# Performance work log

Hardware: AMD Instinct MI355X
Metric: run time of the kernel (lower is better)

Reference implementation:

```python
import jax, jax.numpy as jnp
import numpy as np

MODEL_DIM = 768
N_HEAD = 12
HEAD_DIM = MODEL_DIM // N_HEAD
B, S = 2, 2048


def setup_inputs() -> dict:
    key = jax.random.key(0)
    ks = jax.random.split(key, 11)
    sc = 1.0 / np.sqrt(MODEL_DIM)
    inp = {
        "q": jax.random.normal(ks[0], (B, S, MODEL_DIM), jnp.float32),
        "k": jax.random.normal(ks[1], (B, S, MODEL_DIM), jnp.float32),
        "v": jax.random.normal(ks[2], (B, S, MODEL_DIM), jnp.float32),
        "wq_w": jax.random.normal(ks[3], (MODEL_DIM, MODEL_DIM), jnp.float32) * sc,
        "wq_b": jax.random.normal(ks[4], (MODEL_DIM,), jnp.float32) * sc,
        "wk_w": jax.random.normal(ks[5], (MODEL_DIM, MODEL_DIM), jnp.float32) * sc,
        "wk_b": jax.random.normal(ks[6], (MODEL_DIM,), jnp.float32) * sc,
        "wv_w": jax.random.normal(ks[7], (MODEL_DIM, MODEL_DIM), jnp.float32) * sc,
        "wv_b": jax.random.normal(ks[8], (MODEL_DIM,), jnp.float32) * sc,
        "wo_w": jax.random.normal(ks[9], (MODEL_DIM, MODEL_DIM), jnp.float32) * sc,
        "wo_b": jax.random.normal(ks[10], (MODEL_DIM,), jnp.float32) * sc,
    }
    return inp


def _split_heads(x):
    b, s, _ = x.shape
    return x.reshape(b, s, N_HEAD, HEAD_DIM).transpose(0, 2, 1, 3)  # [B,H,S,Dh]


def reference(q, k, v, wq_w, wq_b, wk_w, wk_b, wv_w, wv_b, wo_w, wo_b):
    # Linear projections (torch Linear: x @ W.T + b)
    query = _split_heads(q @ wq_w.T + wq_b)
    key = _split_heads(k @ wk_w.T + wk_b)
    value = _split_heads(v @ wv_w.T + wv_b)
    scale = 1.0 / np.sqrt(HEAD_DIM)
    scores = jnp.einsum("bhqd,bhkd->bhqk", query, key) * scale
    attn_weights = jax.nn.softmax(scores, axis=-1)
    context = jnp.einsum("bhqk,bhkd->bhqd", attn_weights, value)
    b, h, s, dh = context.shape
    context = context.transpose(0, 2, 1, 3).reshape(b, s, MODEL_DIM)
    output = context @ wo_w.T + wo_b
    return output, attn_weights
```

## Files before the change

### kernel.cpp

```cpp
#include <hip/hip_runtime.h>
#include <stdint.h>

#define S_LEN   2048
#define NH      12
#define NBH     24
#define DMODEL  768
#define OUT0    3145728
#define SD      131072
#define WSZ     589824

#define QB_OFF   0
#define KB_OFF   3145728
#define VB_OFF   6291456
#define WQ_OFF   9437184
#define WK_OFF   10027008
#define WV_OFF   10616832
#define WO_OFF   11206656
#define QH_OFF   11796480
#define KH_OFF   14942208
#define VT_OFF   18087936
#define CTX_OFF  21233664

typedef __attribute__((ext_vector_type(4))) float          f32x4;
typedef __attribute__((ext_vector_type(8))) __bf16         bf16x8;
typedef __attribute__((ext_vector_type(4))) __bf16         bf16x4;
typedef __attribute__((ext_vector_type(4))) float          fl4;
typedef __attribute__((ext_vector_type(4))) unsigned short us4;

__device__ __forceinline__ unsigned short f2bf(float f) {
  union { float f; unsigned u; } x; x.f = f;
  return (unsigned short)((x.u + 0x7FFFu + ((x.u >> 16) & 1u)) >> 16);
}

__device__ __forceinline__ float fexp2(float x) {
#if __has_builtin(__builtin_amdgcn_exp2f)
  return __builtin_amdgcn_exp2f(x);
#else
  return exp2f(x);
#endif
}

__device__ __forceinline__ void gld16(const void* g, void* l) {
  __builtin_amdgcn_global_load_lds((__attribute__((address_space(1))) void*)g,
                                   (__attribute__((address_space(3))) void*)l,
                                   16, 0, 0);
}

#define MFMA(a, b, c) __builtin_amdgcn_mfma_f32_16x16x32_bf16((a), (b), (c), 0, 0, 0)
#define MEMBAR() asm volatile("" ::: "memory")
#define SBAR()   __builtin_amdgcn_s_barrier()

__global__ __launch_bounds__(256) void cvt_kernel(
    const float* __restrict__ q, const float* __restrict__ k, const float* __restrict__ v,
    const float* __restrict__ wq, const float* __restrict__ wk, const float* __restrict__ wv,
    const float* __restrict__ wo, unsigned short* __restrict__ ws)
{
  const int seg = blockIdx.y;
  const float* src; unsigned short* dst; int n; float sc = 1.0f;
  if      (seg == 0) { src = q;  dst = ws + QB_OFF; n = OUT0; }
  else if (seg == 1) { src = k;  dst = ws + KB_OFF; n = OUT0; }
  else if (seg == 2) { src = v;  dst = ws + VB_OFF; n = OUT0; }
  else if (seg == 3) { src = wq; dst = ws + WQ_OFF; n = WSZ; sc = 0.125f; }
  else if (seg == 4) { src = wk; dst = ws + WK_OFF; n = WSZ; }
  else if (seg == 5) { src = wv; dst = ws + WV_OFF; n = WSZ; }
  else               { src = wo; dst = ws + WO_OFF; n = WSZ; }
  const int i4 = blockIdx.x * blockDim.x + threadIdx.x;
  if (i4 * 4 >= n) return;
  fl4 f = ((const fl4*)src)[i4];
  us4 o;
  o.x = f2bf(f.x * sc); o.y = f2bf(f.y * sc);
  o.z = f2bf(f.z * sc); o.w = f2bf(f.w * sc);
  ((us4*)dst)[i4] = o;
}

__global__ __launch_bounds__(256, 2) void proj_qkv(
    unsigned short* __restrict__ ws, const float* __restrict__ bq,
    const float* __restrict__ bk, const float* __restrict__ bv)
{
  __shared__ __align__(16) unsigned short As[2][8192];
  __shared__ __align__(16) unsigned short Bs[2][8192];
  const int mat = blockIdx.z;
  const unsigned short* X = ws + (size_t)mat * OUT0;
  const unsigned short* W = ws + WQ_OFF + (size_t)mat * WSZ;
  const float* bias = (mat == 0) ? bq : ((mat == 1) ? bk : bv);
  const float bsc = (mat == 0) ? 0.125f : 1.0f;
  unsigned short* dst = ws + QH_OFF + (size_t)mat * OUT0;
  const int m0 = blockIdx.y * 128, n0 = blockIdx.x * 128;
  const int tid = threadIdx.x, lane = tid & 63, w = tid >> 6;
  const int wm = w >> 1, wn = w & 1, qd = lane >> 4, ln = lane & 15;
  const int srow = lane >> 3, sc8 = ((lane & 7) ^ srow) * 8;

#pragma unroll
  for (int i = 0; i < 4; i++) {
    const int row = (w * 4 + i) * 8 + srow;
    gld16(X + (size_t)(m0 + row) * 768 + sc8, &As[0][(w * 4 + i) * 512]);
    gld16(W + (size_t)(n0 + row) * 768 + sc8, &Bs[0][(w * 4 + i) * 512]);
  }

  f32x4 acc[4][4] = {};
  for (int kk = 0; kk < 12; kk++) {
    const int knx = (kk == 11) ? 0 : (kk + 1);
    const int nb = (kk + 1) & 1;
#pragma unroll
    for (int i = 0; i < 4; i++) {
      const int row = (w * 4 + i) * 8 + srow;
      gld16(X + (size_t)(m0 + row) * 768 + knx * 64 + sc8, &As[nb][(w * 4 + i) * 512]);
      gld16(W + (size_t)(n0 + row) * 768 + knx * 64 + sc8, &Bs[nb][(w * 4 + i) * 512]);
    }
    asm volatile("s_waitcnt vmcnt(8)" ::: "memory");
    SBAR();
    const unsigned short* Ac = As[kk & 1];
    const unsigned short* Bc = Bs[kk & 1];
    bf16x8 a[4][2], b[4][2];
#pragma unroll
    for (int kst = 0; kst < 2; kst++) {
#pragma unroll
      for (int mt = 0; mt < 4; mt++)
        a[mt][kst] = *(const bf16x8*)(Ac + (wm * 64 + mt * 16 + ln) * 64 + (((kst * 4 + qd) ^ (ln & 7)) * 8));
#pragma unroll
      for (int nt = 0; nt < 4; nt++)
        b[nt][kst] = *(const bf16x8*)(Bc + (wn * 64 + nt * 16 + ln) * 64 + (((kst * 4 + qd) ^ (ln & 7)) * 8));
    }
#pragma unroll
    for (int mt = 0; mt < 4; mt++)
#pragma unroll
      for (int nt = 0; nt < 4; nt++) {
        acc[mt][nt] = MFMA(a[mt][0], b[nt][0], acc[mt][nt]);
        acc[mt][nt] = MFMA(a[mt][1], b[nt][1], acc[mt][nt]);
      }
    MEMBAR();
    SBAR();
  }
#pragma unroll
  for (int nt = 0; nt < 4; nt++) {
    const int n = n0 + wn * 64 + nt * 16 + ln;
    const float bvv = bias[n] * bsc;
    const int h = n >> 6, d = n & 63;
    if (mat < 2) {
#pragma unroll
      for (int mt = 0; mt < 4; mt++)
#pragma unroll
        for (int r = 0; r < 4; r++) {
          const int m = m0 + wm * 64 + mt * 16 + qd * 4 + r;
          const int bb = m >> 11, s = m & 2047;
          dst[(size_t)(bb * NH + h) * SD + (size_t)s * 64 + d] = f2bf(acc[mt][nt][r] + bvv);
        }
    } else {
#pragma unroll
      for (int mt = 0; mt < 4; mt++) {
        const int m = m0 + wm * 64 + mt * 16 + qd * 4;
        const int bb = m >> 11, s = m & 2047;
        us4 o;
        o.x = f2bf(acc[mt][nt][0] + bvv); o.y = f2bf(acc[mt][nt][1] + bvv);
        o.z = f2bf(acc[mt][nt][2] + bvv); o.w = f2bf(acc[mt][nt][3] + bvv);
        *(us4*)(dst + (size_t)(bb * NH + h) * SD + (size_t)d * S_LEN + s) = o;
      }
    }
  }
  asm volatile("s_waitcnt vmcnt(0)" ::: "memory");
}

__global__ __launch_bounds__(256, 2) void attn_kernel(
    unsigned short* __restrict__ ws, float* __restrict__ attn_out)
{
  __shared__ __align__(16) unsigned short lds[40960];
  unsigned short* K0 = lds;
  unsigned short* K1 = lds + 8192;
  unsigned short* Vt = lds + 16384;
  unsigned short* P  = lds + 24576;
  float* rsum        = (float*)(lds + 24576);
  unsigned short* Qs = lds + 32768;

  const int bh = blockIdx.y;
  const int i0 = blockIdx.x * 128;
  const unsigned short* Qg = ws + QH_OFF + (size_t)bh * SD + (size_t)i0 * 64;
  const unsigned short* Kg = ws + KH_OFF + (size_t)bh * SD;
  const unsigned short* Vg = ws + VT_OFF + (size_t)bh * SD;
  float* attnB = attn_out + (size_t)bh * S_LEN * S_LEN + (size_t)i0 * S_LEN;
  unsigned short* ctxB = ws + CTX_OFF + ((size_t)(bh / NH) * S_LEN + i0) * DMODEL + (bh % NH) * 64;

  const int tid = threadIdx.x, lane = tid & 63, w = tid >> 6;
  const int wm = w >> 1, wn = w & 1, qd = lane >> 4, ln = lane & 15;
  const int srow = lane >> 3, sc8 = ((lane & 7) ^ srow) * 8;
  const float LOG2E = 1.4426950408889634f;

#pragma unroll
  for (int i = 0; i < 4; i++) {
    const int row = (w * 4 + i) * 8 + srow;
    gld16(Qg + (size_t)row * 64 + sc8, Qs + (w * 4 + i) * 512);
  }
  MEMBAR();
#pragma unroll
  for (int i = 0; i < 4; i++) {
    const int row = (w * 4 + i) * 8 + srow;
    gld16(Kg + (size_t)row * 64 + sc8, K0 + (w * 4 + i) * 512);
  }
  if (tid < 128) rsum[tid] = 0.f;
  asm volatile("s_waitcnt vmcnt(4) lgkmcnt(0)" ::: "memory");
  SBAR();

  bf16x8 bq[4][2];
#pragma unroll
  for (int kst = 0; kst < 2; kst++)
#pragma unroll
    for (int qt = 0; qt < 4; qt++)
      bq[qt][kst] = *(const bf16x8*)(Qs + (wm * 64 + qt * 16 + ln) * 64 + (((kst * 4 + qd) ^ (ln & 7)) * 8));

  float psl[4] = {0.f, 0.f, 0.f, 0.f};
  for (int jt = 0; jt < 16; jt++) {
    const unsigned short* Kn = Kg + (size_t)((jt + 1) & 15) * 8192;
    unsigned short* Kw = (jt & 1) ? K0 : K1;
#pragma unroll
    for (int i = 0; i < 4; i++) {
      const int row = (w * 4 + i) * 8 + srow;
      gld16(Kn + (size_t)row * 64 + sc8, Kw + (w * 4 + i) * 512);
    }
    asm volatile("s_waitcnt vmcnt(4)" ::: "memory");
    SBAR();
    const unsigned short* Kc = (jt & 1) ? K1 : K0;
    bf16x8 ak[4][2];
#pragma unroll
    for (int kst = 0; kst < 2; kst++)
#pragma unroll
      for (int kt = 0; kt < 4; kt++)
        ak[kt][kst] = *(const bf16x8*)(Kc + (wn * 64 + kt * 16 + ln) * 64 + (((kst * 4 + qd) ^ (ln & 7)) * 8));
#pragma unroll
    for (int qt = 0; qt < 4; qt++)
#pragma unroll
      for (int kt = 0; kt < 4; kt++) {
        f32x4 c = {0.f, 0.f, 0.f, 0.f};
        c = MFMA(ak[kt][0], bq[qt][0], c);
        c = MFMA(ak[kt][1], bq[qt][1], c);
        psl[qt] += fexp2(c[0] * LOG2E) + fexp2(c[1] * LOG2E)
                 + fexp2(c[2] * LOG2E) + fexp2(c[3] * LOG2E);
      }
    MEMBAR();
    SBAR();
  }
#pragma unroll
  for (int qt = 0; qt < 4; qt++) {
    float v = psl[qt];
    v += __shfl_xor(v, 16);
    v += __shfl_xor(v, 32);
    psl[qt] = v;
  }
  if (lane < 16) {
#pragma unroll
    for (int qt = 0; qt < 4; qt++)
      atomicAdd(&rsum[wm * 64 + qt * 16 + lane], psl[qt]);
  }
  asm volatile("s_waitcnt lgkmcnt(0)" ::: "memory");
  SBAR();
  float rv[4];
#pragma unroll
  for (int qt = 0; qt < 4; qt++) rv[qt] = 1.0f / rsum[wm * 64 + qt * 16 + ln];

  f32x4 ctx[4][2] = {};
  for (int jt = 0; jt < 16; jt++) {
#pragma unroll
    for (int i = 0; i < 4; i++) {
      const int d = (w * 4 + i) * 4 + qd;
      const int csw = ((lane & 15) ^ ((i & 1) * 4 + qd)) * 8;
      gld16(Vg + (size_t)d * S_LEN + jt * 128 + csw, Vt + (w * 4 + i) * 512);
    }
    MEMBAR();
    const unsigned short* Kn = Kg + (size_t)((jt + 1) & 15) * 8192;
    unsigned short* Kw = (jt & 1) ? K0 : K1;
#pragma unroll
    for (int i = 0; i < 4; i++) {
      const int row = (w * 4 + i) * 8 + srow;
      gld16(Kn + (size_t)row * 64 + sc8, Kw + (w * 4 + i) * 512);
    }
    asm volatile("s_waitcnt vmcnt(8)" ::: "memory");
    SBAR();

    const unsigned short* Kc = (jt & 1) ? K1 : K0;
    bf16x8 ak[4][2];
#pragma unroll
    for (int kst = 0; kst < 2; kst++)
#pragma unroll
      for (int kt = 0; kt < 4; kt++)
        ak[kt][kst] = *(const bf16x8*)(Kc + (wn * 64 + kt * 16 + ln) * 64 + (((kst * 4 + qd) ^ (ln & 7)) * 8));

#pragma unroll
    for (int qt = 0; qt < 4; qt++) {
      const int qrow = wm * 64 + qt * 16 + ln;
      float* aRow = attnB + (size_t)qrow * S_LEN + jt * 128 + wn * 64 + qd * 4;
      unsigned short* pRow = P + qrow * 128;
      const int r7x8 = (ln & 7) * 8;
#pragma unroll
      for (int kt = 0; kt < 4; kt++) {
        f32x4 c = {0.f, 0.f, 0.f, 0.f};
        c = MFMA(ak[kt][0], bq[qt][0], c);
        c = MFMA(ak[kt][1], bq[qt][1], c);
        f32x4 pv;
        pv.x = fexp2(c[0] * LOG2E) * rv[qt];
        pv.y = fexp2(c[1] * LOG2E) * rv[qt];
        pv.z = fexp2(c[2] * LOG2E) * rv[qt];
        pv.w = fexp2(c[3] * LOG2E) * rv[qt];
        *(f32x4*)(aRow + kt * 16) = pv;
        bf16x4 pb;
        pb.x = (__bf16)pv.x; pb.y = (__bf16)pv.y;
        pb.z = (__bf16)pv.z; pb.w = (__bf16)pv.w;
        *(bf16x4*)(pRow + ((wn * 64 + kt * 16 + qd * 4) ^ r7x8)) = pb;
      }
    }
    asm volatile("s_waitcnt vmcnt(20) lgkmcnt(0)" ::: "memory");
    SBAR();
#pragma unroll
    for (int kst = 0; kst < 4; kst++) {
      bf16x8 pa[4], vb[2];
#pragma unroll
      for (int mt = 0; mt < 4; mt++)
        pa[mt] = *(const bf16x8*)(P + (wm * 64 + mt * 16 + ln) * 128 + ((kst * 32 + qd * 8) ^ ((ln & 7) * 8)));
#pragma unroll
      for (int nt = 0; nt < 2; nt++)
        vb[nt] = *(const bf16x8*)(Vt + (wn * 32 + nt * 16 + ln) * 128 + (((kst * 4 + qd) ^ (ln & 7)) * 8));
#pragma unroll
      for (int mt = 0; mt < 4; mt++)
#pragma unroll
        for (int nt = 0; nt < 2; nt++)
          ctx[mt][nt] = MFMA(pa[mt], vb[nt], ctx[mt][nt]);
    }
    MEMBAR();
    SBAR();
  }
#pragma unroll
  for (int mt = 0; mt < 4; mt++)
#pragma unroll
    for (int nt = 0; nt < 2; nt++)
#pragma unroll
      for (int r = 0; r < 4; r++) {
        const int row = wm * 64 + mt * 16 + qd * 4 + r;
        ctxB[(size_t)row * DMODEL + wn * 32 + nt * 16 + ln] = f2bf(ctx[mt][nt][r]);
      }
  asm volatile("s_waitcnt vmcnt(0)" ::: "memory");
}

__global__ __launch_bounds__(256, 2) void out_proj(
    const unsigned short* __restrict__ ws, const float* __restrict__ wob,
    float* __restrict__ out)
{
  __shared__ __align__(16) unsigned short As[2][8192];
  __shared__ __align__(16) unsigned short Bs[2][8192];
  const unsigned short* X = ws + CTX_OFF;
  const unsigned short* W = ws + WO_OFF;
  const int m0 = blockIdx.y * 128, n0 = blockIdx.x * 128;
  const int tid = threadIdx.x, lane = tid & 63, w = tid >> 6;
  const int wm = w >> 1, wn = w & 1, qd = lane >> 4, ln = lane & 15;
  const int srow = lane >> 3, sc8 = ((lane & 7) ^ srow) * 8;

#pragma unroll
  for (int i = 0; i < 4; i++) {
    const int row = (w * 4 + i) * 8 + srow;
    gld16(X + (size_t)(m0 + row) * 768 + sc8, &As[0][(w * 4 + i) * 512]);
    gld16(W + (size_t)(n0 + row) * 768 + sc8, &Bs[0][(w * 4 + i) * 512]);
  }

  f32x4 acc[4][4] = {};
  for (int kk = 0; kk < 12; kk++) {
    const int knx = (kk == 11) ? 0 : (kk + 1);
    const int nb = (kk + 1) & 1;
#pragma unroll
    for (int i = 0; i < 4; i++) {
      const int row = (w * 4 + i) * 8 + srow;
      gld16(X + (size_t)(m0 + row) * 768 + knx * 64 + sc8, &As[nb][(w * 4 + i) * 512]);
      gld16(W + (size_t)(n0 + row) * 768 + knx * 64 + sc8, &Bs[nb][(w * 4 + i) * 512]);
    }
    asm volatile("s_waitcnt vmcnt(8)" ::: "memory");
    SBAR();
    const unsigned short* Ac = As[kk & 1];
    const unsigned short* Bc = Bs[kk & 1];
    bf16x8 a[4][2], b[4][2];
#pragma unroll
    for (int kst = 0; kst < 2; kst++) {
#pragma unroll
      for (int mt = 0; mt < 4; mt++)
        a[mt][kst] = *(const bf16x8*)(Ac + (wm * 64 + mt * 16 + ln) * 64 + (((kst * 4 + qd) ^ (ln & 7)) * 8));
#pragma unroll
      for (int nt = 0; nt < 4; nt++)
        b[nt][kst] = *(const bf16x8*)(Bc + (wn * 64 + nt * 16 + ln) * 64 + (((kst * 4 + qd) ^ (ln & 7)) * 8));
    }
#pragma unroll
    for (int mt = 0; mt < 4; mt++)
#pragma unroll
      for (int nt = 0; nt < 4; nt++) {
        acc[mt][nt] = MFMA(a[mt][0], b[nt][0], acc[mt][nt]);
        acc[mt][nt] = MFMA(a[mt][1], b[nt][1], acc[mt][nt]);
      }
    MEMBAR();
    SBAR();
  }
#pragma unroll
  for (int nt = 0; nt < 4; nt++) {
    const int n = n0 + wn * 64 + nt * 16 + ln;
    const float bvv = wob[n];
#pragma unroll
    for (int mt = 0; mt < 4; mt++)
#pragma unroll
      for (int r = 0; r < 4; r++) {
        const int m = m0 + wm * 64 + mt * 16 + qd * 4 + r;
        out[(size_t)m * DMODEL + n] = acc[mt][nt][r] + bvv;
      }
  }
  asm volatile("s_waitcnt vmcnt(0)" ::: "memory");
}

extern "C" void kernel_launch(void* const* d_in, const int* in_sizes, int n_in,
                              void* d_out, int out_size, void* d_ws, size_t ws_size,
                              hipStream_t stream)
{
  const float* q  = (const float*)d_in[0];
  const float* k  = (const float*)d_in[1];
  const float* v  = (const float*)d_in[2];
  const float* wq = (const float*)d_in[3];
  const float* bq = (const float*)d_in[4];
  const float* wk = (const float*)d_in[5];
  const float* bk = (const float*)d_in[6];
  const float* wv = (const float*)d_in[7];
  const float* bv = (const float*)d_in[8];
  const float* wo = (const float*)d_in[9];
  const float* bo = (const float*)d_in[10];
  unsigned short* ws = (unsigned short*)d_ws;
  float* out = (float*)d_out;

  cvt_kernel<<<dim3(3072, 7), 256, 0, stream>>>(q, k, v, wq, wk, wv, wo, ws);
  proj_qkv<<<dim3(6, 32, 3), 256, 0, stream>>>(ws, bq, bk, bv);
  attn_kernel<<<dim3(16, 24), 256, 0, stream>>>(ws, out + OUT0);
  out_proj<<<dim3(6, 32), 256, 0, stream>>>(ws, bo, out);
}
```

Baseline: 569.0 us.

## Shrink attention tile to 64 query rows and keep P in registers via shuffles

The attention kernel now processes 64 query rows per block instead of 128. Each wave owns 16 full query rows, so row sums reduce within the wave without LDS atomics. The softmax probabilities are packed to bf16 in registers and redistributed with cross-lane shuffles into the MFMA A-operand layout, which removes the P staging buffer in LDS. Q is staged in the Vt buffer, LDS drops from 80KB to 48KB, and launch bounds rise to 3 blocks per CU to raise occupancy. In exchange, each K/V tile loaded from global memory is reused by fewer query rows, doubling K/V traffic, and the kernel adds shuffle overhead.

```diff
diff --git a/kernel.cpp b/kernel.cpp
--- a/kernel.cpp
+++ b/kernel.cpp
@@ -23,7 +23,6 @@
 
 typedef __attribute__((ext_vector_type(4))) float          f32x4;
 typedef __attribute__((ext_vector_type(8))) __bf16         bf16x8;
-typedef __attribute__((ext_vector_type(4))) __bf16         bf16x4;
 typedef __attribute__((ext_vector_type(4))) float          fl4;
 typedef __attribute__((ext_vector_type(4))) unsigned short us4;
 
@@ -160,19 +159,16 @@
   asm volatile("s_waitcnt vmcnt(0)" ::: "memory");
 }
 
-__global__ __launch_bounds__(256, 2) void attn_kernel(
+__global__ __launch_bounds__(256, 3) void attn_kernel(
     unsigned short* __restrict__ ws, float* __restrict__ attn_out)
 {
-  __shared__ __align__(16) unsigned short lds[40960];
+  __shared__ __align__(16) unsigned short lds[24576];
   unsigned short* K0 = lds;
   unsigned short* K1 = lds + 8192;
   unsigned short* Vt = lds + 16384;
-  unsigned short* P  = lds + 24576;
-  float* rsum        = (float*)(lds + 24576);
-  unsigned short* Qs = lds + 32768;
 
   const int bh = blockIdx.y;
-  const int i0 = blockIdx.x * 128;
+  const int i0 = blockIdx.x * 64;
   const unsigned short* Qg = ws + QH_OFF + (size_t)bh * SD + (size_t)i0 * 64;
   const unsigned short* Kg = ws + KH_OFF + (size_t)bh * SD;
   const unsigned short* Vg = ws + VT_OFF + (size_t)bh * SD;
@@ -180,14 +176,14 @@
   unsigned short* ctxB = ws + CTX_OFF + ((size_t)(bh / NH) * S_LEN + i0) * DMODEL + (bh % NH) * 64;
 
   const int tid = threadIdx.x, lane = tid & 63, w = tid >> 6;
-  const int wm = w >> 1, wn = w & 1, qd = lane >> 4, ln = lane & 15;
+  const int qd = lane >> 4, ln = lane & 15;
   const int srow = lane >> 3, sc8 = ((lane & 7) ^ srow) * 8;
   const float LOG2E = 1.4426950408889634f;
 
 #pragma unroll
-  for (int i = 0; i < 4; i++) {
-    const int row = (w * 4 + i) * 8 + srow;
-    gld16(Qg + (size_t)row * 64 + sc8, Qs + (w * 4 + i) * 512);
+  for (int i = 0; i < 2; i++) {
+    const int row = (w * 2 + i) * 8 + srow;
+    gld16(Qg + (size_t)row * 64 + sc8, Vt + (w * 2 + i) * 512);
   }
   MEMBAR();
 #pragma unroll
@@ -195,21 +191,18 @@
     const int row = (w * 4 + i) * 8 + srow;
     gld16(Kg + (size_t)row * 64 + sc8, K0 + (w * 4 + i) * 512);
   }
-  if (tid < 128) rsum[tid] = 0.f;
-  asm volatile("s_waitcnt vmcnt(4) lgkmcnt(0)" ::: "memory");
+  asm volatile("s_waitcnt vmcnt(4)" ::: "memory");
   SBAR();
 
-  bf16x8 bq[4][2];
+  bf16x8 bq[2];
 #pragma unroll
   for (int kst = 0; kst < 2; kst++)
-#pragma unroll
-    for (int qt = 0; qt < 4; qt++)
-      bq[qt][kst] = *(const bf16x8*)(Qs + (wm * 64 + qt * 16 + ln) * 64 + (((kst * 4 + qd) ^ (ln & 7)) * 8));
-
-  float psl[4] = {0.f, 0.f, 0.f, 0.f};
+    bq[kst] = *(const bf16x8*)(Vt + (w * 16 + ln) * 64 + (((kst * 4 + qd) ^ (ln & 7)) * 8));
+
+  float psl = 0.f;
   for (int jt = 0; jt < 16; jt++) {
     const unsigned short* Kn = Kg + (size_t)((jt + 1) & 15) * 8192;
-    unsigned short* Kw = (jt & 1) ? K0 : K1;
+    unsigned short* Kw = ((jt + 1) & 1) ? K1 : K0;
 #pragma unroll
     for (int i = 0; i < 4; i++) {
       const int row = (w * 4 + i) * 8 + srow;
@@ -218,44 +211,28 @@
     asm volatile("s_waitcnt vmcnt(4)" ::: "memory");
     SBAR();
     const unsigned short* Kc = (jt & 1) ? K1 : K0;
-    bf16x8 ak[4][2];
-#pragma unroll
-    for (int kst = 0; kst < 2; kst++)
-#pragma unroll
-      for (int kt = 0; kt < 4; kt++)
-        ak[kt][kst] = *(const bf16x8*)(Kc + (wn * 64 + kt * 16 + ln) * 64 + (((kst * 4 + qd) ^ (ln & 7)) * 8));
-#pragma unroll
-    for (int qt = 0; qt < 4; qt++)
-#pragma unroll
-      for (int kt = 0; kt < 4; kt++) {
-        f32x4 c = {0.f, 0.f, 0.f, 0.f};
-        c = MFMA(ak[kt][0], bq[qt][0], c);
-        c = MFMA(ak[kt][1], bq[qt][1], c);
-        psl[qt] += fexp2(c[0] * LOG2E) + fexp2(c[1] * LOG2E)
-                 + fexp2(c[2] * LOG2E) + fexp2(c[3] * LOG2E);
-      }
-    MEMBAR();
-    SBAR();
-  }
-#pragma unroll
-  for (int qt = 0; qt < 4; qt++) {
-    float v = psl[qt];
-    v += __shfl_xor(v, 16);
-    v += __shfl_xor(v, 32);
-    psl[qt] = v;
-  }
-  if (lane < 16) {
-#pragma unroll
-    for (int qt = 0; qt < 4; qt++)
-      atomicAdd(&rsum[wm * 64 + qt * 16 + lane], psl[qt]);
-  }
-  asm volatile("s_waitcnt lgkmcnt(0)" ::: "memory");
-  SBAR();
-  float rv[4];
-#pragma unroll
-  for (int qt = 0; qt < 4; qt++) rv[qt] = 1.0f / rsum[wm * 64 + qt * 16 + ln];
-
-  f32x4 ctx[4][2] = {};
+#pragma unroll
+    for (int kt = 0; kt < 8; kt++) {
+      bf16x8 ak0 = *(const bf16x8*)(Kc + (kt * 16 + ln) * 64 + ((qd ^ (ln & 7)) * 8));
+      bf16x8 ak1 = *(const bf16x8*)(Kc + (kt * 16 + ln) * 64 + (((4 + qd) ^ (ln & 7)) * 8));
+      f32x4 c = {0.f, 0.f, 0.f, 0.f};
+      c = MFMA(ak0, bq[0], c);
+      c = MFMA(ak1, bq[1], c);
+      psl += fexp2(c[0] * LOG2E) + fexp2(c[1] * LOG2E)
+           + fexp2(c[2] * LOG2E) + fexp2(c[3] * LOG2E);
+    }
+    MEMBAR();
+    SBAR();
+  }
+  psl += __shfl_xor(psl, 16);
+  psl += __shfl_xor(psl, 32);
+  const float rv = 1.0f / psl;
+
+  const int l0 = ((qd & 1) * 2) * 16 + ln;
+  const int l1 = l0 + 16;
+  const bool hi = (qd & 2) != 0;
+
+  f32x4 ctx[4] = {};
   for (int jt = 0; jt < 16; jt++) {
 #pragma unroll
     for (int i = 0; i < 4; i++) {
@@ -265,7 +242,7 @@
     }
     MEMBAR();
     const unsigned short* Kn = Kg + (size_t)((jt + 1) & 15) * 8192;
-    unsigned short* Kw = (jt & 1) ? K0 : K1;
+    unsigned short* Kw = ((jt + 1) & 1) ? K1 : K0;
 #pragma unroll
     for (int i = 0; i < 4; i++) {
       const int row = (w * 4 + i) * 8 + srow;
@@ -275,65 +252,52 @@
     SBAR();
 
     const unsigned short* Kc = (jt & 1) ? K1 : K0;
-    bf16x8 ak[4][2];
-#pragma unroll
-    for (int kst = 0; kst < 2; kst++)
-#pragma unroll
-      for (int kt = 0; kt < 4; kt++)
-        ak[kt][kst] = *(const bf16x8*)(Kc + (wn * 64 + kt * 16 + ln) * 64 + (((kst * 4 + qd) ^ (ln & 7)) * 8));
-
-#pragma unroll
-    for (int qt = 0; qt < 4; qt++) {
-      const int qrow = wm * 64 + qt * 16 + ln;
-      float* aRow = attnB + (size_t)qrow * S_LEN + jt * 128 + wn * 64 + qd * 4;
-      unsigned short* pRow = P + qrow * 128;
-      const int r7x8 = (ln & 7) * 8;
-#pragma unroll
-      for (int kt = 0; kt < 4; kt++) {
-        f32x4 c = {0.f, 0.f, 0.f, 0.f};
-        c = MFMA(ak[kt][0], bq[qt][0], c);
-        c = MFMA(ak[kt][1], bq[qt][1], c);
-        f32x4 pv;
-        pv.x = fexp2(c[0] * LOG2E) * rv[qt];
-        pv.y = fexp2(c[1] * LOG2E) * rv[qt];
-        pv.z = fexp2(c[2] * LOG2E) * rv[qt];
-        pv.w = fexp2(c[3] * LOG2E) * rv[qt];
-        *(f32x4*)(aRow + kt * 16) = pv;
-        bf16x4 pb;
-        pb.x = (__bf16)pv.x; pb.y = (__bf16)pv.y;
-        pb.z = (__bf16)pv.z; pb.w = (__bf16)pv.w;
-        *(bf16x4*)(pRow + ((wn * 64 + kt * 16 + qd * 4) ^ r7x8)) = pb;
-      }
-    }
-    asm volatile("s_waitcnt vmcnt(20) lgkmcnt(0)" ::: "memory");
-    SBAR();
+    unsigned pkx[8], pky[8];
+#pragma unroll
+    for (int kt = 0; kt < 8; kt++) {
+      bf16x8 ak0 = *(const bf16x8*)(Kc + (kt * 16 + ln) * 64 + ((qd ^ (ln & 7)) * 8));
+      bf16x8 ak1 = *(const bf16x8*)(Kc + (kt * 16 + ln) * 64 + (((4 + qd) ^ (ln & 7)) * 8));
+      f32x4 c = {0.f, 0.f, 0.f, 0.f};
+      c = MFMA(ak0, bq[0], c);
+      c = MFMA(ak1, bq[1], c);
+      f32x4 pv;
+      pv.x = fexp2(c[0] * LOG2E) * rv;
+      pv.y = fexp2(c[1] * LOG2E) * rv;
+      pv.z = fexp2(c[2] * LOG2E) * rv;
+      pv.w = fexp2(c[3] * LOG2E) * rv;
+      *(f32x4*)(attnB + (size_t)(w * 16 + ln) * S_LEN + jt * 128 + kt * 16 + qd * 4) = pv;
+      pkx[kt] = (unsigned)f2bf(pv.x) | ((unsigned)f2bf(pv.y) << 16);
+      pky[kt] = (unsigned)f2bf(pv.z) | ((unsigned)f2bf(pv.w) << 16);
+    }
+    asm volatile("s_waitcnt vmcnt(12)" ::: "memory");
+    SBAR();
+
 #pragma unroll
     for (int kst = 0; kst < 4; kst++) {
-      bf16x8 pa[4], vb[2];
-#pragma unroll
-      for (int mt = 0; mt < 4; mt++)
-        pa[mt] = *(const bf16x8*)(P + (wm * 64 + mt * 16 + ln) * 128 + ((kst * 32 + qd * 8) ^ ((ln & 7) * 8)));
-#pragma unroll
-      for (int nt = 0; nt < 2; nt++)
-        vb[nt] = *(const bf16x8*)(Vt + (wn * 32 + nt * 16 + ln) * 128 + (((kst * 4 + qd) ^ (ln & 7)) * 8));
-#pragma unroll
-      for (int mt = 0; mt < 4; mt++)
-#pragma unroll
-        for (int nt = 0; nt < 2; nt++)
-          ctx[mt][nt] = MFMA(pa[mt], vb[nt], ctx[mt][nt]);
-    }
-    MEMBAR();
-    SBAR();
-  }
-#pragma unroll
-  for (int mt = 0; mt < 4; mt++)
-#pragma unroll
-    for (int nt = 0; nt < 2; nt++)
-#pragma unroll
-      for (int r = 0; r < 4; r++) {
-        const int row = wm * 64 + mt * 16 + qd * 4 + r;
-        ctxB[(size_t)row * DMODEL + wn * 32 + nt * 16 + ln] = f2bf(ctx[mt][nt][r]);
-      }
+      const int kA = kst * 2, kB = kst * 2 + 1;
+      const int t0a = __shfl((int)pkx[kA], l0), t1a = __shfl((int)pky[kA], l0);
+      const int t2a = __shfl((int)pkx[kA], l1), t3a = __shfl((int)pky[kA], l1);
+      const int t0b = __shfl((int)pkx[kB], l0), t1b = __shfl((int)pky[kB], l0);
+      const int t2b = __shfl((int)pkx[kB], l1), t3b = __shfl((int)pky[kB], l1);
+      union { int u[4]; bf16x8 v; } pw;
+      pw.u[0] = hi ? t0b : t0a; pw.u[1] = hi ? t1b : t1a;
+      pw.u[2] = hi ? t2b : t2a; pw.u[3] = hi ? t3b : t3a;
+#pragma unroll
+      for (int nt = 0; nt < 4; nt++) {
+        bf16x8 vb = *(const bf16x8*)(Vt + (nt * 16 + ln) * 128 + (((kst * 4 + qd) ^ (ln & 7)) * 8));
+        ctx[nt] = MFMA(pw.v, vb, ctx[nt]);
+      }
+    }
+    MEMBAR();
+    SBAR();
+  }
+#pragma unroll
+  for (int nt = 0; nt < 4; nt++)
+#pragma unroll
+    for (int r = 0; r < 4; r++) {
+      const int row = w * 16 + qd * 4 + r;
+      ctxB[(size_t)row * DMODEL + nt * 16 + ln] = f2bf(ctx[nt][r]);
+    }
   asm volatile("s_waitcnt vmcnt(0)" ::: "memory");
 }
 
@@ -426,6 +390,6 @@
 
   cvt_kernel<<<dim3(3072, 7), 256, 0, stream>>>(q, k, v, wq, wk, wv, wo, ws);
   proj_qkv<<<dim3(6, 32, 3), 256, 0, stream>>>(ws, bq, bk, bv);
-  attn_kernel<<<dim3(16, 24), 256, 0, stream>>>(ws, out + OUT0);
+  attn_kernel<<<dim3(32, 24), 256, 0, stream>>>(ws, out + OUT0);
   out_proj<<<dim3(6, 32), 256, 0, stream>>>(ws, bo, out);
 }
```

New measurement: 568.8 us. Within noise of the previous version (-0.0%).
